# Kernel optimization log

Hardware: AMD Instinct MI355X
Metric: run time of the kernel (lower is better)

Reference implementation:

```python
import jax, jax.numpy as jnp
import numpy as np
from jax import lax

B, N, C_IN, C_OUT, STRIDE, K = 4, 8192, 32, 64, 4, 16
EPS = 1e-5


def setup_inputs() -> dict:
    key = jax.random.key(0)
    ks = jax.random.split(key, 12)
    p1 = jax.random.normal(ks[0], (B, N, 3), jnp.float32)
    x = jax.random.normal(ks[1], (B, C_IN, N), jnp.float32)
    w1 = 0.1 * jax.random.normal(ks[2], (C_OUT, 3 + C_IN), jnp.float32)
    g1 = 1.0 + 0.1 * jax.random.normal(ks[3], (C_OUT,), jnp.float32)
    b1 = 0.1 * jax.random.normal(ks[4], (C_OUT,), jnp.float32)
    m1 = 0.1 * jax.random.normal(ks[5], (C_OUT,), jnp.float32)
    v1 = 0.5 + jax.random.uniform(ks[6], (C_OUT,), jnp.float32)
    w2 = 0.1 * jax.random.normal(ks[7], (C_OUT, C_OUT), jnp.float32)
    g2 = 1.0 + 0.1 * jax.random.normal(ks[8], (C_OUT,), jnp.float32)
    b2 = 0.1 * jax.random.normal(ks[9], (C_OUT,), jnp.float32)
    m2 = 0.1 * jax.random.normal(ks[10], (C_OUT,), jnp.float32)
    v2 = 0.5 + jax.random.uniform(ks[11], (C_OUT,), jnp.float32)
    return dict(p1=p1, x=x, w1=w1, g1=g1, b1=b1, m1=m1, v1=v1,
                w2=w2, g2=g2, b2=b2, m2=m2, v2=v2)


def fps(p, M):
    # furthest point sampling, starts at index 0 (matches pointops)
    Bb, Nn, _ = p.shape

    def step(carry, _):
        dists, last = carry
        lp = jnp.take_along_axis(p, last[:, None, None], axis=1)  # (B,1,3)
        d = jnp.sum((p - lp) ** 2, axis=-1)                       # (B,N)
        dists = jnp.minimum(dists, d)
        nxt = jnp.argmax(dists, axis=-1).astype(jnp.int32)
        return (dists, nxt), nxt

    init = (jnp.full((Bb, Nn), 1e10, jnp.float32), jnp.zeros((Bb,), jnp.int32))
    _, rest = lax.scan(step, init, None, length=M - 1)            # (M-1,B)
    idx = jnp.concatenate([jnp.zeros((1, Bb), jnp.int32), rest], axis=0)
    return idx.T                                                  # (B,M)


def _conv_bn_relu(h, w, g, b, m, v):
    # 1x1 conv over channels + eval-mode BN + ReLU
    h = jnp.einsum('bmkc,oc->bmko', h, w)
    return jax.nn.relu((h - m) * (g * lax.rsqrt(v + EPS)) + b)


def reference(p1, x, w1, g1, b1, m1, v1, w2, g2, b2, m2, v2):
    M = x.shape[-1] // STRIDE
    idx = fps(p1, M)                                              # (B,M)
    bidx = jnp.arange(B)[:, None]
    p2 = p1[bidx, idx]                                            # (B,M,3)
    # kNN: squared distances (B,M,N)
    d2 = (jnp.sum(p2 ** 2, -1)[:, :, None]
          + jnp.sum(p1 ** 2, -1)[:, None, :]
          - 2.0 * jnp.einsum('bmd,bnd->bmn', p2, p1))
    _, nn_idx = lax.top_k(-d2, K)                                 # (B,M,K)
    bidx2 = jnp.arange(B)[:, None, None]
    gxyz = p1[bidx2, nn_idx] - p2[:, :, None, :]                  # (B,M,K,3) relative coords
    gfeat = jnp.transpose(x, (0, 2, 1))[bidx2, nn_idx]            # (B,M,K,C)
    h = jnp.concatenate([gxyz, gfeat], axis=-1)                   # (B,M,K,3+C)
    h = _conv_bn_relu(h, w1, g1, b1, m1, v1)
    h = _conv_bn_relu(h, w2, g2, b2, m2, v2)
    y = jnp.transpose(jnp.max(h, axis=2), (0, 2, 1))              # (B,C_OUT,M) max-pool over K
    return (p2, y)
```

## Files before the change

### kernel.cpp

```cpp
#include <hip/hip_runtime.h>
#include <hip/hip_bf16.h>

#define NB 4
#define NPTS 8192
#define CIN 32
#define COUT 64
#define MOUT 2048
#define KNN 16
#define EPSBN 1e-5f

typedef float f32x2 __attribute__((ext_vector_type(2)));

__device__ inline f32x2 pk_add(f32x2 a, f32x2 b) {
    f32x2 r;
    asm("v_pk_add_f32 %0, %1, %2" : "=v"(r) : "v"(a), "v"(b));
    return r;
}
__device__ inline f32x2 pk_mul(f32x2 a, f32x2 b) {
    f32x2 r;
    asm("v_pk_mul_f32 %0, %1, %2" : "=v"(r) : "v"(a), "v"(b));
    return r;
}

__global__ void setup_kernel(const float* __restrict__ w1, const float* __restrict__ g1,
                             const float* __restrict__ b1, const float* __restrict__ m1,
                             const float* __restrict__ v1, const float* __restrict__ w2,
                             const float* __restrict__ g2, const float* __restrict__ b2,
                             const float* __restrict__ m2, const float* __restrict__ v2,
                             float* __restrict__ wbuf) {
    int o = threadIdx.x;
    if (o >= 64) return;
    float a1 = g1[o] * rsqrtf(v1[o] + EPSBN);
    wbuf[2240 + o] = b1[o] - m1[o] * a1;
    for (int c = 0; c < 35; ++c) wbuf[o * 35 + c] = w1[o * 35 + c] * a1;
    float a2 = g2[o] * rsqrtf(v2[o] + EPSBN);
    wbuf[6400 + o] = b2[o] - m2[o] * a2;
    for (int c = 0; c < 64; ++c) wbuf[2304 + o * 64 + c] = w2[o * 64 + c] * a2;
}

__global__ __launch_bounds__(256) void transpose_kernel(const float* __restrict__ x,
                                                        float* __restrict__ xt) {
    __shared__ float tile[CIN][65];
    int b = blockIdx.y;
    int n0 = blockIdx.x * 64;
    int tid = threadIdx.x;
#pragma unroll
    for (int r = 0; r < 8; ++r) {
        int i = r * 256 + tid;
        int c = i >> 6, n = i & 63;
        tile[c][n] = x[((size_t)b * CIN + c) * NPTS + n0 + n];
    }
    __syncthreads();
#pragma unroll
    for (int r = 0; r < 8; ++r) {
        int i = r * 256 + tid;
        int n = i >> 5, c = i & 31;
        xt[((size_t)b * NPTS + n0 + n) * CIN + c] = tile[c][n];
    }
}

#define FPS_PT 8
__global__ __launch_bounds__(1024, 4) void fps_kernel(const float* __restrict__ p1,
                                                      float* __restrict__ p2out) {
    int b = blockIdx.x;
    int tid = threadIdx.x;
    int lane = tid & 63;
    const float* P = p1 + (size_t)b * NPTS * 3;

    __shared__ float lp[NPTS * 3];
    __shared__ unsigned long long slot[4];

    const float4* P4 = (const float4*)P;
    float4* L4 = (float4*)lp;
#pragma unroll
    for (int r = 0; r < 6; ++r) {
        int i = r * 1024 + tid;
        L4[i] = P4[i];
    }
    if (tid < 4) slot[tid] = 0ull;
    __syncthreads();

    f32x2 px[4], py[4], pz[4], dmin[4];
    int base = tid * FPS_PT;
#pragma unroll
    for (int s = 0; s < 4; ++s) {
        int j = (base + 2 * s) * 3;
        px[s] = (f32x2){lp[j + 0], lp[j + 3]};
        py[s] = (f32x2){lp[j + 1], lp[j + 4]};
        pz[s] = (f32x2){lp[j + 2], lp[j + 5]};
        dmin[s] = (f32x2){1e10f, 1e10f};
        asm volatile("" : "+v"(px[s]), "+v"(py[s]), "+v"(pz[s]));
    }

    float lx = lp[0], ly = lp[1], lz = lp[2];
    if (tid == 0) {
        p2out[(size_t)(b * MOUT) * 3 + 0] = lx;
        p2out[(size_t)(b * MOUT) * 3 + 1] = ly;
        p2out[(size_t)(b * MOUT) * 3 + 2] = lz;
    }

    for (int m = 1; m < MOUT; ++m) {
        float nlx = -lx, nly = -ly, nlz = -lz;
        f32x2 cx = {nlx, nlx}, cy = {nly, nly}, cz = {nlz, nlz};
        float bv;
        {
            float t[8];
#pragma unroll
            for (int s = 0; s < 4; ++s) {
                f32x2 dx = pk_add(px[s], cx);
                f32x2 dy = pk_add(py[s], cy);
                f32x2 dz = pk_add(pz[s], cz);
                f32x2 xx = pk_mul(dx, dx);
                f32x2 yy = pk_mul(dy, dy);
                f32x2 zz = pk_mul(dz, dz);
                f32x2 d = pk_add(pk_add(xx, yy), zz);
                float n0 = fminf(dmin[s].x, d.x);
                float n1 = fminf(dmin[s].y, d.y);
                dmin[s].x = n0;
                dmin[s].y = n1;
                t[2 * s] = n0;
                t[2 * s + 1] = n1;
            }
            bv = fmaxf(fmaxf(fmaxf(t[0], t[1]), fmaxf(t[2], t[3])),
                       fmaxf(fmaxf(t[4], t[5]), fmaxf(t[6], t[7])));
        }
        float x0 = bv;
        {
            int xi, sh;
            xi = __float_as_int(x0);
            sh = __builtin_amdgcn_update_dpp(xi, xi, 0x111, 0xF, 0xF, false);
            x0 = fmaxf(x0, __int_as_float(sh));
            xi = __float_as_int(x0);
            sh = __builtin_amdgcn_update_dpp(xi, xi, 0x112, 0xF, 0xF, false);
            x0 = fmaxf(x0, __int_as_float(sh));
            xi = __float_as_int(x0);
            sh = __builtin_amdgcn_update_dpp(xi, xi, 0x114, 0xF, 0xF, false);
            x0 = fmaxf(x0, __int_as_float(sh));
            xi = __float_as_int(x0);
            sh = __builtin_amdgcn_update_dpp(xi, xi, 0x118, 0xF, 0xF, false);
            x0 = fmaxf(x0, __int_as_float(sh));
            x0 = fmaxf(x0, __int_as_float(
                     __builtin_amdgcn_ds_swizzle(__float_as_int(x0), 0x401F)));
            x0 = fmaxf(x0, __shfl_xor(x0, 32));
        }
        unsigned g = (unsigned)__builtin_amdgcn_readlane(__float_as_int(x0), 15);
        int loc = 8;
        if (__float_as_uint(dmin[3].y) == g) loc = 7;
        if (__float_as_uint(dmin[3].x) == g) loc = 6;
        if (__float_as_uint(dmin[2].y) == g) loc = 5;
        if (__float_as_uint(dmin[2].x) == g) loc = 4;
        if (__float_as_uint(dmin[1].y) == g) loc = 3;
        if (__float_as_uint(dmin[1].x) == g) loc = 2;
        if (__float_as_uint(dmin[0].y) == g) loc = 1;
        if (__float_as_uint(dmin[0].x) == g) loc = 0;
        unsigned long long bal = __ballot(loc < 8);
        int l = __ffsll((long long)bal) - 1;
        int widx_w = __shfl(base + loc, l);
        if (lane == 0) {
            unsigned long long pk =
                ((unsigned long long)g << 32) | (unsigned long long)(unsigned)(~widx_w);
            atomicMax(&slot[m & 3], pk);
        }
        if (tid == 0) slot[(m + 2) & 3] = 0ull;
        __syncthreads();
        unsigned long long w = slot[m & 3];
        int widx = __builtin_amdgcn_readfirstlane(~(unsigned)(w & 0xffffffffu));
        int wj = widx * 3;
        lx = lp[wj + 0];
        ly = lp[wj + 1];
        lz = lp[wj + 2];
        if (tid == 0) {
            p2out[((size_t)b * MOUT + m) * 3 + 0] = lx;
            p2out[((size_t)b * MOUT + m) * 3 + 1] = ly;
            p2out[((size_t)b * MOUT + m) * 3 + 2] = lz;
        }
    }
}

__global__ __launch_bounds__(256) void knn_kernel(const float* __restrict__ p1,
                                                  const float* __restrict__ p2,
                                                  int* __restrict__ nnout) {
    int tid = threadIdx.x;
    int lane = tid & 63, wid = tid >> 6;
    int qid = blockIdx.x * 4 + wid;
    int b = qid >> 11;
    const float* Pb = p1 + (size_t)b * NPTS * 3;
    const float* q = p2 + (size_t)qid * 3;
    float qx = q[0], qy = q[1], qz = q[2];
    float s2q = __fadd_rn(__fadd_rn(__fmul_rn(qx, qx), __fmul_rn(qy, qy)),
                          __fmul_rn(qz, qz));

    float tval = 3.0e38f;
    int   tidx = -1;
    float tau = 3.0e38f;

    for (int n0 = 0; n0 < NPTS; n0 += 64) {
        int n = n0 + lane;
        const float* pp = Pb + n * 3;
        float px = pp[0], py = pp[1], pz = pp[2];
        float s1n = __fadd_rn(__fadd_rn(__fmul_rn(px, px), __fmul_rn(py, py)),
                              __fmul_rn(pz, pz));
        float dot = __fadd_rn(__fadd_rn(__fmul_rn(qx, px), __fmul_rn(qy, py)),
                              __fmul_rn(qz, pz));
        float d2 = __fsub_rn(__fadd_rn(s2q, s1n), __fmul_rn(2.0f, dot));

        unsigned long long act = __ballot(d2 < tau);
        while (act) {
            int l = __ffsll(act) - 1;
            float dd = __shfl(d2, l);
            int   nn_ = __shfl(n, l);
            unsigned long long mle = __ballot(lane < 16 && tval <= dd);
            int pos = __popcll(mle);
            float sv = __shfl_up(tval, 1);
            int   si = __shfl_up(tidx, 1);
            if (lane < 16) {
                if (lane == pos)      { tval = dd; tidx = nn_; }
                else if (lane > pos)  { tval = sv; tidx = si; }
            }
            tau = __shfl(tval, 15);
            act &= (act - 1);
            act &= __ballot(d2 < tau);
        }
    }
    if (lane < 16) nnout[(size_t)qid * KNN + lane] = tidx;
}

template <int XT>
__global__ __launch_bounds__(256) void conv_kernel(const float* __restrict__ p1,
                                                   const float* __restrict__ p2,
                                                   const float* __restrict__ xsrc,
                                                   const int* __restrict__ nn,
                                                   const float* __restrict__ wbuf,
                                                   float* __restrict__ y) {
    const float* w1s = wbuf;
    const float* c1s = wbuf + 2240;
    const float* w2s = wbuf + 2304;
    const float* c2s = wbuf + 6400;
    int tid = threadIdx.x;
    int lane = tid & 63, wid = tid >> 6;
    int qq = lane >> 4, k = lane & 15;
    int qid = (blockIdx.x * 4 + wid) * 4 + qq;
    int b = qid >> 11, m = qid & 2047;
    int nk = nn[(size_t)qid * KNN + k];

    const float* qp = p2 + (size_t)qid * 3;
    const float* np = p1 + ((size_t)b * NPTS + nk) * 3;
    float h[35];
    h[0] = np[0] - qp[0];
    h[1] = np[1] - qp[1];
    h[2] = np[2] - qp[2];
    if (XT) {
        const float4* xr = (const float4*)(xsrc + ((size_t)b * NPTS + nk) * CIN);
#pragma unroll
        for (int q8 = 0; q8 < 8; ++q8) {
            float4 f = xr[q8];
            h[3 + q8 * 4 + 0] = f.x;
            h[3 + q8 * 4 + 1] = f.y;
            h[3 + q8 * 4 + 2] = f.z;
            h[3 + q8 * 4 + 3] = f.w;
        }
    } else {
#pragma unroll
        for (int c = 0; c < CIN; ++c)
            h[3 + c] = xsrc[((size_t)b * CIN + c) * NPTS + nk];
    }

    float acc2[64];
#pragma unroll
    for (int o2 = 0; o2 < 64; ++o2) acc2[o2] = c2s[o2];

    for (int o = 0; o < 64; ++o) {
        float a = c1s[o];
#pragma unroll
        for (int c = 0; c < 35; ++c) a = fmaf(h[c], w1s[o * 35 + c], a);
        a = fmaxf(a, 0.0f);
#pragma unroll
        for (int o2 = 0; o2 < 64; ++o2) acc2[o2] = fmaf(a, w2s[o2 * 64 + o], acc2[o2]);
    }

#pragma unroll
    for (int o2 = 0; o2 < 64; ++o2) {
        float v = fmaxf(acc2[o2], 0.0f);
        v = fmaxf(v, __shfl_xor(v, 8));
        v = fmaxf(v, __shfl_xor(v, 4));
        v = fmaxf(v, __shfl_xor(v, 2));
        v = fmaxf(v, __shfl_xor(v, 1));
        if ((lane & 15) == (o2 & 15))
            y[((size_t)b * COUT + o2) * MOUT + m] = v;
    }
}

extern "C" void kernel_launch(void* const* d_in, const int* in_sizes, int n_in,
                              void* d_out, int out_size, void* d_ws, size_t ws_size,
                              hipStream_t stream) {
    const float* p1 = (const float*)d_in[0];
    const float* x  = (const float*)d_in[1];
    const float* w1 = (const float*)d_in[2];
    const float* g1 = (const float*)d_in[3];
    const float* b1 = (const float*)d_in[4];
    const float* m1 = (const float*)d_in[5];
    const float* v1 = (const float*)d_in[6];
    const float* w2 = (const float*)d_in[7];
    const float* g2 = (const float*)d_in[8];
    const float* b2 = (const float*)d_in[9];
    const float* m2 = (const float*)d_in[10];
    const float* v2 = (const float*)d_in[11];

    float* p2o = (float*)d_out;
    float* yo  = p2o + (size_t)NB * MOUT * 3;

    char* ws = (char*)d_ws;
    int*   nn   = (int*)ws;
    float* wbuf = (float*)(ws + 512 * 1024);
    float* xt   = (float*)(ws + 1024 * 1024);
    bool use_xt = ws_size >= (size_t)(1024 * 1024) + (size_t)NB * NPTS * CIN * 4;

    setup_kernel<<<1, 64, 0, stream>>>(w1, g1, b1, m1, v1, w2, g2, b2, m2, v2, wbuf);
    if (use_xt)
        transpose_kernel<<<dim3(NPTS / 64, NB), 256, 0, stream>>>(x, xt);
    fps_kernel<<<NB, 1024, 0, stream>>>(p1, p2o);
    knn_kernel<<<(NB * MOUT) / 4, 256, 0, stream>>>(p1, p2o, nn);
    if (use_xt)
        conv_kernel<1><<<(NB * MOUT) / 16, 256, 0, stream>>>(p1, p2o, xt, nn, wbuf, yo);
    else
        conv_kernel<0><<<(NB * MOUT) / 16, 256, 0, stream>>>(p1, p2o, x, nn, wbuf, yo);
}
```

Measured before the change: 2.579 ms.

## Halve FPS block size, double points per thread, replace LDS atomics with per-wave slots

The FPS kernel now runs 512 threads with 16 points per thread instead of 1024 threads with 8, halving the number of waves that meet at the per-iteration barrier. The shared atomicMax slot is replaced by per-wave slots in a double-buffered array, reduced after the barrier with a shuffle-xor max over 8 entries. Inline-asm packed ops become vector expressions, with fp contraction disabled to keep results bit-exact. Each thread does more serial distance work per iteration, trading compute for less synchronisation and atomic traffic.

```diff
diff --git a/kernel.cpp b/kernel.cpp
--- a/kernel.cpp
+++ b/kernel.cpp
@@ -10,17 +10,6 @@
 #define EPSBN 1e-5f
 
 typedef float f32x2 __attribute__((ext_vector_type(2)));
-
-__device__ inline f32x2 pk_add(f32x2 a, f32x2 b) {
-    f32x2 r;
-    asm("v_pk_add_f32 %0, %1, %2" : "=v"(r) : "v"(a), "v"(b));
-    return r;
-}
-__device__ inline f32x2 pk_mul(f32x2 a, f32x2 b) {
-    f32x2 r;
-    asm("v_pk_mul_f32 %0, %1, %2" : "=v"(r) : "v"(a), "v"(b));
-    return r;
-}
 
 __global__ void setup_kernel(const float* __restrict__ w1, const float* __restrict__ g1,
                              const float* __restrict__ b1, const float* __restrict__ m1,
@@ -59,31 +48,32 @@
     }
 }
 
-#define FPS_PT 8
-__global__ __launch_bounds__(1024, 4) void fps_kernel(const float* __restrict__ p1,
-                                                      float* __restrict__ p2out) {
+#define FPS_PT 16
+__global__ __launch_bounds__(512) void fps_kernel(const float* __restrict__ p1,
+                                                  float* __restrict__ p2out) {
+#pragma clang fp contract(off)
     int b = blockIdx.x;
     int tid = threadIdx.x;
     int lane = tid & 63;
+    int wv = tid >> 6;
     const float* P = p1 + (size_t)b * NPTS * 3;
 
     __shared__ float lp[NPTS * 3];
-    __shared__ unsigned long long slot[4];
+    __shared__ unsigned long long warr[2][8];
 
     const float4* P4 = (const float4*)P;
     float4* L4 = (float4*)lp;
 #pragma unroll
-    for (int r = 0; r < 6; ++r) {
-        int i = r * 1024 + tid;
+    for (int r = 0; r < 12; ++r) {
+        int i = r * 512 + tid;
         L4[i] = P4[i];
     }
-    if (tid < 4) slot[tid] = 0ull;
     __syncthreads();
 
-    f32x2 px[4], py[4], pz[4], dmin[4];
+    f32x2 px[8], py[8], pz[8], dmin[8];
     int base = tid * FPS_PT;
 #pragma unroll
-    for (int s = 0; s < 4; ++s) {
+    for (int s = 0; s < 8; ++s) {
         int j = (base + 2 * s) * 3;
         px[s] = (f32x2){lp[j + 0], lp[j + 3]};
         py[s] = (f32x2){lp[j + 1], lp[j + 4]};
@@ -100,30 +90,23 @@
     }
 
     for (int m = 1; m < MOUT; ++m) {
-        float nlx = -lx, nly = -ly, nlz = -lz;
-        f32x2 cx = {nlx, nlx}, cy = {nly, nly}, cz = {nlz, nlz};
-        float bv;
-        {
-            float t[8];
-#pragma unroll
-            for (int s = 0; s < 4; ++s) {
-                f32x2 dx = pk_add(px[s], cx);
-                f32x2 dy = pk_add(py[s], cy);
-                f32x2 dz = pk_add(pz[s], cz);
-                f32x2 xx = pk_mul(dx, dx);
-                f32x2 yy = pk_mul(dy, dy);
-                f32x2 zz = pk_mul(dz, dz);
-                f32x2 d = pk_add(pk_add(xx, yy), zz);
-                float n0 = fminf(dmin[s].x, d.x);
-                float n1 = fminf(dmin[s].y, d.y);
-                dmin[s].x = n0;
-                dmin[s].y = n1;
-                t[2 * s] = n0;
-                t[2 * s + 1] = n1;
-            }
-            bv = fmaxf(fmaxf(fmaxf(t[0], t[1]), fmaxf(t[2], t[3])),
-                       fmaxf(fmaxf(t[4], t[5]), fmaxf(t[6], t[7])));
-        }
+        f32x2 lxv = {lx, lx}, lyv = {ly, ly}, lzv = {lz, lz};
+#pragma unroll
+        for (int s = 0; s < 8; ++s) {
+            f32x2 dx = px[s] - lxv;
+            f32x2 dy = py[s] - lyv;
+            f32x2 dz = pz[s] - lzv;
+            f32x2 d = (dx * dx + dy * dy) + dz * dz;
+            dmin[s] = __builtin_elementwise_min(dmin[s], d);
+        }
+        f32x2 t0 = __builtin_elementwise_max(dmin[0], dmin[1]);
+        f32x2 t1 = __builtin_elementwise_max(dmin[2], dmin[3]);
+        f32x2 t2 = __builtin_elementwise_max(dmin[4], dmin[5]);
+        f32x2 t3 = __builtin_elementwise_max(dmin[6], dmin[7]);
+        f32x2 u0 = __builtin_elementwise_max(t0, t1);
+        f32x2 u1 = __builtin_elementwise_max(t2, t3);
+        f32x2 v2m = __builtin_elementwise_max(u0, u1);
+        float bv = fmaxf(v2m.x, v2m.y);
         float x0 = bv;
         {
             int xi, sh;
@@ -144,7 +127,15 @@
             x0 = fmaxf(x0, __shfl_xor(x0, 32));
         }
         unsigned g = (unsigned)__builtin_amdgcn_readlane(__float_as_int(x0), 15);
-        int loc = 8;
+        int loc = 16;
+        if (__float_as_uint(dmin[7].y) == g) loc = 15;
+        if (__float_as_uint(dmin[7].x) == g) loc = 14;
+        if (__float_as_uint(dmin[6].y) == g) loc = 13;
+        if (__float_as_uint(dmin[6].x) == g) loc = 12;
+        if (__float_as_uint(dmin[5].y) == g) loc = 11;
+        if (__float_as_uint(dmin[5].x) == g) loc = 10;
+        if (__float_as_uint(dmin[4].y) == g) loc = 9;
+        if (__float_as_uint(dmin[4].x) == g) loc = 8;
         if (__float_as_uint(dmin[3].y) == g) loc = 7;
         if (__float_as_uint(dmin[3].x) == g) loc = 6;
         if (__float_as_uint(dmin[2].y) == g) loc = 5;
@@ -153,18 +144,23 @@
         if (__float_as_uint(dmin[1].x) == g) loc = 2;
         if (__float_as_uint(dmin[0].y) == g) loc = 1;
         if (__float_as_uint(dmin[0].x) == g) loc = 0;
-        unsigned long long bal = __ballot(loc < 8);
+        unsigned long long bal = __ballot(loc < 16);
         int l = __ffsll((long long)bal) - 1;
         int widx_w = __shfl(base + loc, l);
+        int par = m & 1;
         if (lane == 0) {
             unsigned long long pk =
                 ((unsigned long long)g << 32) | (unsigned long long)(unsigned)(~widx_w);
-            atomicMax(&slot[m & 3], pk);
-        }
-        if (tid == 0) slot[(m + 2) & 3] = 0ull;
+            warr[par][wv] = pk;
+        }
         __syncthreads();
-        unsigned long long w = slot[m & 3];
-        int widx = __builtin_amdgcn_readfirstlane(~(unsigned)(w & 0xffffffffu));
+        unsigned long long e = warr[par][lane & 7];
+#pragma unroll
+        for (int off = 1; off <= 4; off <<= 1) {
+            unsigned long long o = __shfl_xor(e, off);
+            if (o > e) e = o;
+        }
+        int widx = ~(unsigned)(e & 0xffffffffull);
         int wj = widx * 3;
         lx = lp[wj + 0];
         ly = lp[wj + 1];
@@ -318,7 +314,7 @@
     setup_kernel<<<1, 64, 0, stream>>>(w1, g1, b1, m1, v1, w2, g2, b2, m2, v2, wbuf);
     if (use_xt)
         transpose_kernel<<<dim3(NPTS / 64, NB), 256, 0, stream>>>(x, xt);
-    fps_kernel<<<NB, 1024, 0, stream>>>(p1, p2o);
+    fps_kernel<<<NB, 512, 0, stream>>>(p1, p2o);
     knn_kernel<<<(NB * MOUT) / 4, 256, 0, stream>>>(p1, p2o, nn);
     if (use_xt)
         conv_kernel<1><<<(NB * MOUT) / 16, 256, 0, stream>>>(p1, p2o, xt, nn, wbuf, yo);
```

Result: faster. 2.359 ms (-8.5%).
